# Performance work log

Measured on AMD Instinct MI355X. Metric: run time of the kernel, lower is better.

The kernel has to match this reference:

```python
import jax, jax.numpy as jnp
import numpy as np

N_ENT = 50000
N_REL = 1000
D_E = 32
D_R = 32
RANK = 40
B = 64
EPS = 1e-5


def _bn(x, gamma, beta):
    # BatchNorm1d in training mode: biased batch stats over the batch dim
    mu = x.mean(axis=0)
    var = x.var(axis=0)
    return (x - mu) * jax.lax.rsqrt(var + EPS) * gamma + beta


def setup_inputs() -> dict:
    key = jax.random.key(0)
    ks = jax.random.split(key, 10)
    E_weight = jax.random.normal(ks[0], (N_ENT, D_E), jnp.float32) * 0.001
    E_weight = E_weight.at[0].set(0.0)  # padding_idx=0
    R_weight = jax.random.normal(ks[1], (N_REL, D_R), jnp.float32) * 0.001
    R_weight = R_weight.at[0].set(0.0)
    ht_left = jax.random.normal(ks[2], (RANK, D_E, D_E), jnp.float32) * 0.1
    ht_right = jax.random.normal(ks[3], (RANK, D_E, D_E), jnp.float32) * 0.1
    ht_internal = jax.random.normal(ks[4], (RANK, RANK, RANK), jnp.float32) * 0.1
    ht_root = jax.random.normal(ks[5], (D_R, RANK), jnp.float32) * 0.1
    r_idx = jax.random.randint(ks[6], (B,), 0, N_REL)
    e_idx = jax.random.randint(ks[7], (3, B), 0, N_ENT)
    return {
        "E_weight": E_weight, "R_weight": R_weight,
        "ht_left": ht_left, "ht_right": ht_right,
        "ht_internal": ht_internal, "ht_root": ht_root,
        "bne_gamma": jnp.ones(D_E), "bne_beta": jnp.zeros(D_E),
        "bnr_gamma": jnp.ones(D_R), "bnr_beta": jnp.zeros(D_R),
        "bnw_gamma": jnp.ones(D_E), "bnw_beta": jnp.zeros(D_E),
        "r_idx": r_idx, "e_idx": e_idx, "miss_ent_domain": 1,
    }


def reference(E_weight, R_weight, ht_left, ht_right, ht_internal, ht_root,
              bne_gamma, bne_beta, bnr_gamma, bnr_beta, bnw_gamma, bnw_beta,
              r_idx, e_idx, miss_ent_domain):
    d_r = R_weight.shape[1]
    d_e = E_weight.shape[1]
    # build_W: HT contraction to full 5-D core W[d,i,j,k,l]
    W_int = jnp.einsum('cab,aij,bkl->cijkl', ht_internal, ht_left, ht_right)
    W = jnp.einsum('dc,cijkl->dijkl', ht_root, W_int)
    # relation-conditioned core
    r_emb = _bn(R_weight[r_idx], bnr_gamma, bnr_beta)           # [B, d_r]
    W_mat = (r_emb @ W.reshape(d_r, -1)).reshape(-1, d_e, d_e, d_e, d_e)
    # known entity embeddings (dropout = 0)
    es = [_bn(E_weight[e_idx[i]], bne_gamma, bne_beta) for i in range(3)]
    eq = {1: 'bijkl,bj,bk,bl->bi', 2: 'bijkl,bi,bk,bl->bj',
          3: 'bijkl,bi,bj,bl->bk', 4: 'bijkl,bi,bj,bk->bl'}[int(miss_ent_domain)]
    W_out = jnp.einsum(eq, W_mat, *es)                          # [B, d_e]
    W_out = _bn(W_out, bnw_gamma, bnw_beta)
    pred = jax.nn.softmax(W_out @ E_weight.T, axis=1)           # [B, n_ent]
    return (pred, W)
```

## Files before the change

### kernel.cpp

```cpp
#include <hip/hip_runtime.h>

#define N_ENT 50000
#define D_E 32
#define RANK 40
#define NB 64
#define EPS 1e-5f

#define GN (32 * RANK * RANK)
#define GBLK ((GN + 255) / 256)
#define WBLK 1024
#define LBLK ((N_ENT + 255) / 256)
#define NXCH 25

typedef float f32x4 __attribute__((ext_vector_type(4)));


__global__ __launch_bounds__(256) void k_prep(
    const float* __restrict__ Ew, const float* __restrict__ Rw,
    const float* __restrict__ L, const float* __restrict__ Rt,
    const float* __restrict__ internal, const float* __restrict__ root,
    const float* __restrict__ bne_g, const float* __restrict__ bne_b,
    const float* __restrict__ bnr_g, const float* __restrict__ bnr_b,
    const int* __restrict__ r_idx, const int* __restrict__ e_idx,
    const int* __restrict__ dom_p,
    float* __restrict__ G, float* __restrict__ wraw)
{
    int t = threadIdx.x;
    int blk = blockIdx.x;
    if (blk >= NB) {
        int idx = (blk - NB) * 256 + t;
        if (idx < GN) {
            int d  = idx / (RANK * RANK);
            int ab = idx - d * (RANK * RANK);
            float acc = 0.f;
            #pragma unroll 8
            for (int c = 0; c < RANK; ++c)
                acc += root[d * RANK + c] * internal[c * RANK * RANK + ab];
            G[idx] = acc;
        }
        return;
    }
    int bb = blk;
    int dom = *dom_p;
    __shared__ float sTab[4][NB][32];
    __shared__ float sMu[4][32], sRs[4][32], sBt[4][32];
    __shared__ float sRow[4][32];
    __shared__ float sRc_[RANK];
    __shared__ float sGr[RANK * RANK];
    __shared__ float sv[RANK], sg[RANK];
    __shared__ float sX[RANK * 32];

    for (int e = t; e < NB * 32; e += 256) {
        int r = e >> 5, c = e & 31;
        sTab[0][r][c] = Rw[r_idx[r] * 32 + c];
        sTab[1][r][c] = Ew[(size_t)e_idx[r] * 32 + c];
        sTab[2][r][c] = Ew[(size_t)e_idx[NB + r] * 32 + c];
        sTab[3][r][c] = Ew[(size_t)e_idx[2 * NB + r] * 32 + c];
    }
    __syncthreads();
    if (t < 128) {
        int tb = t >> 5, c = t & 31;
        float s = 0.f;
        for (int r = 0; r < NB; ++r) s += sTab[tb][r][c];
        float mean = s * (1.f / NB);
        float v = 0.f;
        for (int r = 0; r < NB; ++r) { float d = sTab[tb][r][c] - mean; v += d * d; }
        v *= (1.f / NB);
        const float* gm = (tb == 0) ? bnr_g : bne_g;
        const float* bt = (tb == 0) ? bnr_b : bne_b;
        sMu[tb][c] = mean;
        sRs[tb][c] = gm[c] / sqrtf(v + EPS);
        sBt[tb][c] = bt[c];
    }
    __syncthreads();
    if (t < 128) {
        int tb = t >> 5, c = t & 31;
        sRow[tb][c] = (sTab[tb][bb][c] - sMu[tb][c]) * sRs[tb][c] + sBt[tb][c];
    }
    __syncthreads();
    if (t < RANK) {
        float acc = 0.f;
        #pragma unroll 8
        for (int d = 0; d < 32; ++d) acc += sRow[0][d] * root[d * RANK + t];
        sRc_[t] = acc;
    }
    const float* s0 = sRow[1];
    const float* s1 = sRow[2];
    const float* s2 = sRow[3];
    if (dom <= 2) {
        if (t < RANK) {
            float acc = 0.f;
            for (int k = 0; k < 32; ++k) {
                float inner = 0.f;
                #pragma unroll 8
                for (int l = 0; l < 32; ++l) inner += Rt[t * 1024 + k * 32 + l] * s2[l];
                acc += inner * s1[k];
            }
            sv[t] = acc;
        }
        for (int e = t; e < RANK * 32; e += 256) {
            int a = e >> 5, o = e & 31;
            float acc = 0.f;
            if (dom == 1) { for (int j = 0; j < 32; ++j) acc += L[a * 1024 + o * 32 + j] * s0[j]; }
            else          { for (int i = 0; i < 32; ++i) acc += L[a * 1024 + i * 32 + o] * s0[i]; }
            sX[e] = acc;
        }
    } else {
        if (t < RANK) {
            float acc = 0.f;
            for (int i = 0; i < 32; ++i) {
                float inner = 0.f;
                #pragma unroll 8
                for (int j = 0; j < 32; ++j) inner += L[t * 1024 + i * 32 + j] * s1[j];
                acc += inner * s0[i];
            }
            sv[t] = acc;
        }
        for (int e = t; e < RANK * 32; e += 256) {
            int b2 = e >> 5, o = e & 31;
            float acc = 0.f;
            if (dom == 3) { for (int l = 0; l < 32; ++l) acc += Rt[b2 * 1024 + o * 32 + l] * s2[l]; }
            else          { for (int k = 0; k < 32; ++k) acc += Rt[b2 * 1024 + k * 32 + o] * s1[k]; }
            sX[e] = acc;
        }
    }
    __syncthreads();
    for (int e = t; e < RANK * RANK; e += 256) {
        float acc = 0.f;
        #pragma unroll 8
        for (int c = 0; c < RANK; ++c) acc += sRc_[c] * internal[c * RANK * RANK + e];
        sGr[e] = acc;
    }
    __syncthreads();
    if (t < RANK) {
        float acc = 0.f;
        if (dom <= 2) { for (int b2 = 0; b2 < RANK; ++b2) acc += sGr[t * RANK + b2] * sv[b2]; }
        else          { for (int a = 0; a < RANK; ++a)   acc += sGr[a * RANK + t] * sv[a]; }
        sg[t] = acc;
    }
    __syncthreads();
    if (t < 32) {
        float acc = 0.f;
        for (int x = 0; x < RANK; ++x) acc += sg[x] * sX[x * 32 + t];
        wraw[bb * 32 + t] = acc;
    }
}

__global__ __launch_bounds__(256) void k_main(
    const float* __restrict__ G, const float* __restrict__ L,
    const float* __restrict__ Rt, const float* __restrict__ E,
    const float* __restrict__ wraw,
    const float* __restrict__ bnw_g, const float* __restrict__ bnw_b,
    float* __restrict__ W, float* __restrict__ pred, float* __restrict__ psum)
{
    __shared__ float smem[6400];
    int t = threadIdx.x;
    if (blockIdx.x < WBLK) {
        float* sT  = smem;
        float* sRc = smem + 1280;
        int blk = blockIdx.x, d = blk >> 5, i = blk & 31;
        for (int e = t; e < RANK * 32; e += 256) {
            int b2 = e >> 5, j = e & 31;
            float acc = 0.f;
            #pragma unroll 8
            for (int a = 0; a < RANK; ++a)
                acc += G[d * (RANK * RANK) + a * RANK + b2] * L[a * 1024 + i * 32 + j];
            sT[b2 * 32 + j] = acc;
        }
        int jg  = (t >> 5) << 2;
        int kq4 = (t & 31) << 2;
        float* Wrow = W + (size_t)blk * 32 * 1024;
        const f32x4* R4 = (const f32x4*)Rt;
        f32x4* sRc4 = (f32x4*)sRc;
        for (int ch = 0; ch < 8; ++ch) {
            __syncthreads();
            for (int e = t; e < RANK * 32; e += 256) {
                int b2 = e >> 5, x = e & 31;
                sRc4[b2 * 32 + x] = R4[b2 * 256 + ch * 32 + x];
            }
            __syncthreads();
            float acc[4][4] = {};
            #pragma unroll 4
            for (int b2 = 0; b2 < RANK; ++b2) {
                f32x4 tv = *(const f32x4*)&sT[b2 * 32 + jg];
                f32x4 rv = *(const f32x4*)&sRc[b2 * 128 + kq4];
                acc[0][0] += tv.x * rv.x; acc[0][1] += tv.x * rv.y; acc[0][2] += tv.x * rv.z; acc[0][3] += tv.x * rv.w;
                acc[1][0] += tv.y * rv.x; acc[1][1] += tv.y * rv.y; acc[1][2] += tv.y * rv.z; acc[1][3] += tv.y * rv.w;
                acc[2][0] += tv.z * rv.x; acc[2][1] += tv.z * rv.y; acc[2][2] += tv.z * rv.z; acc[2][3] += tv.z * rv.w;
                acc[3][0] += tv.w * rv.x; acc[3][1] += tv.w * rv.y; acc[3][2] += tv.w * rv.z; acc[3][3] += tv.w * rv.w;
            }
            #pragma unroll
            for (int jy = 0; jy < 4; ++jy) {
                f32x4 o = { acc[jy][0], acc[jy][1], acc[jy][2], acc[jy][3] };
                __builtin_nontemporal_store(o, (f32x4*)&Wrow[(size_t)(jg + jy) * 1024 + ch * 128 + kq4]);
            }
        }
    } else {
        int chunk = blockIdx.x - WBLK;
        float* wbn  = smem;
        float* sacc = smem + 2048;
        float* sst  = smem + 2304;
        for (int e = t; e < 2048; e += 256) wbn[e] = wraw[e];
        __syncthreads();
        if (t < 32) {
            float s = 0.f;
            for (int r = 0; r < NB; ++r) s += wbn[r * 32 + t];
            float mean = s * (1.f / NB);
            float v = 0.f;
            for (int r = 0; r < NB; ++r) { float d = wbn[r * 32 + t] - mean; v += d * d; }
            v *= (1.f / NB);
            sst[t]      = mean;
            sst[32 + t] = bnw_g[t] / sqrtf(v + EPS);
            sst[64 + t] = bnw_b[t];
        }
        __syncthreads();
        for (int e = t; e < 2048; e += 256) {
            int c = e & 31;
            wbn[e] = (wbn[e] - sst[c]) * sst[32 + c] + sst[64 + c];
        }
        __syncthreads();
        int ent = chunk * 256 + t;
        bool valid = ent < N_ENT;
        float er[32];
        if (valid) {
            const f32x4* Er = (const f32x4*)(E + (size_t)ent * 32);
            #pragma unroll
            for (int q = 0; q < 8; ++q) {
                f32x4 v4 = Er[q];
                er[q * 4 + 0] = v4.x; er[q * 4 + 1] = v4.y;
                er[q * 4 + 2] = v4.z; er[q * 4 + 3] = v4.w;
            }
        } else {
            #pragma unroll
            for (int q = 0; q < 32; ++q) er[q] = 0.f;
        }
        int wv = t >> 6;
        for (int b = 0; b < NB; ++b) {
            float s = 0.f;
            #pragma unroll
            for (int p = 0; p < 32; ++p) s += wbn[b * 32 + p] * er[p];
            if (valid) pred[(size_t)b * N_ENT + ent] = s;
            float pz = valid ? __expf(s) : 0.f;
            #pragma unroll
            for (int off = 32; off >= 1; off >>= 1) pz += __shfl_xor(pz, off);
            if ((t & 63) == 0) sacc[wv * 64 + b] = pz;
        }
        __syncthreads();
        if (t < NB)
            psum[chunk * NB + t] = sacc[t] + sacc[64 + t] + sacc[128 + t] + sacc[192 + t];
    }
}

__global__ __launch_bounds__(256) void k_normexp(
    float* __restrict__ pred, const float* __restrict__ psum)
{
    int b = blockIdx.y, cx = blockIdx.x, t = threadIdx.x;
    __shared__ float sred[4];
    __shared__ float sinv;
    float v = (t < LBLK) ? psum[t * NB + b] : 0.f;
    #pragma unroll
    for (int off = 32; off >= 1; off >>= 1) v += __shfl_xor(v, off);
    if ((t & 63) == 0) sred[t >> 6] = v;
    __syncthreads();
    if (t == 0) sinv = 1.f / (sred[0] + sred[1] + sred[2] + sred[3]);
    __syncthreads();
    float inv = sinv;
    f32x4* p4 = (f32x4*)pred + (size_t)b * (N_ENT / 4);
    #pragma unroll
    for (int q = 0; q < 2; ++q) {
        int f = cx * 512 + q * 256 + t;
        if (f < N_ENT / 4) {
            f32x4 x = p4[f];
            x.x = __expf(x.x) * inv; x.y = __expf(x.y) * inv;
            x.z = __expf(x.z) * inv; x.w = __expf(x.w) * inv;
            p4[f] = x;
        }
    }
}

extern "C" void kernel_launch(void* const* d_in, const int* in_sizes, int n_in,
                              void* d_out, int out_size, void* d_ws, size_t ws_size,
                              hipStream_t stream) {
    const float* E_weight = (const float*)d_in[0];
    const float* R_weight = (const float*)d_in[1];
    const float* ht_left  = (const float*)d_in[2];
    const float* ht_right = (const float*)d_in[3];
    const float* ht_int   = (const float*)d_in[4];
    const float* ht_root  = (const float*)d_in[5];
    const float* bne_g = (const float*)d_in[6];
    const float* bne_b = (const float*)d_in[7];
    const float* bnr_g = (const float*)d_in[8];
    const float* bnr_b = (const float*)d_in[9];
    const float* bnw_g = (const float*)d_in[10];
    const float* bnw_b = (const float*)d_in[11];
    const int* r_idx = (const int*)d_in[12];
    const int* e_idx = (const int*)d_in[13];
    const int* dom   = (const int*)d_in[14];

    float* ws   = (float*)d_ws;
    float* G    = ws;
    float* wraw = ws + 51200;
    float* psum = ws + 53248;

    float* pred = (float*)d_out;
    float* Wout = (float*)d_out + (size_t)NB * N_ENT;

    k_prep<<<NB + GBLK, 256, 0, stream>>>(E_weight, R_weight, ht_left, ht_right,
                                          ht_int, ht_root, bne_g, bne_b, bnr_g, bnr_b,
                                          r_idx, e_idx, dom, G, wraw);
    k_main<<<WBLK + LBLK, 256, 0, stream>>>(G, ht_left, ht_right, E_weight, wraw,
                                            bnw_g, bnw_b, Wout, pred, psum);
    {
        dim3 g(NXCH, NB);
        k_normexp<<<g, 256, 0, stream>>>(pred, psum);
    }
}
```

Baseline: 122.2 us.

## Build W with bf16 MFMA and recompute logits instead of storing pred twice

The W core is now formed with 32x32x16 bf16 MFMA instructions. The ht_right factor is pre-packed into a bf16 fragment layout in the prep kernel, and the per-block T tile is converted to bf16 in shared memory. The softmax path no longer writes raw logits and reads them back. The middle kernel only produces exp partial sums, and a final kernel recomputes the logits from E, applies exp and normalisation, and writes pred once. This removes a full read-modify-write of the 12.8MB pred array, at the cost of recomputing the dot products and reducing W's precision to bf16 inputs, which may exceed the tolerance.

```diff
diff --git a/kernel.cpp b/kernel.cpp
--- a/kernel.cpp
+++ b/kernel.cpp
@@ -1,19 +1,26 @@
 #include <hip/hip_runtime.h>
 
 #define N_ENT 50000
-#define D_E 32
 #define RANK 40
 #define NB 64
 #define EPS 1e-5f
 
 #define GN (32 * RANK * RANK)
-#define GBLK ((GN + 255) / 256)
+#define GBLK 200
+#define RFBLK 32
 #define WBLK 1024
-#define LBLK ((N_ENT + 255) / 256)
-#define NXCH 25
-
-typedef float f32x4 __attribute__((ext_vector_type(4)));
-
+#define LBLK 196
+
+typedef float f32x4  __attribute__((ext_vector_type(4)));
+typedef float f32x16 __attribute__((ext_vector_type(16)));
+typedef short s16x8  __attribute__((ext_vector_type(8)));
+
+
+__device__ __forceinline__ unsigned short f2bf(float f) {
+    unsigned u = __float_as_uint(f);
+    u += 0x7FFF + ((u >> 16) & 1);
+    return (unsigned short)(u >> 16);
+}
 
 __global__ __launch_bounds__(256) void k_prep(
     const float* __restrict__ Ew, const float* __restrict__ Rw,
@@ -23,10 +30,24 @@
     const float* __restrict__ bnr_g, const float* __restrict__ bnr_b,
     const int* __restrict__ r_idx, const int* __restrict__ e_idx,
     const int* __restrict__ dom_p,
-    float* __restrict__ G, float* __restrict__ wraw)
+    float* __restrict__ G, float* __restrict__ wraw,
+    unsigned short* __restrict__ RfU)
 {
     int t = threadIdx.x;
     int blk = blockIdx.x;
+    if (blk >= NB + GBLK) {
+        int nt = blk - (NB + GBLK);
+        for (int e = t; e < 1536; e += 256) {
+            int i  = e & 7;
+            int l  = (e >> 3) & 63;
+            int ks = e >> 9;
+            int b  = 16 * ks + 8 * (l >> 5) + i;
+            int n  = nt * 32 + (l & 31);
+            float v = (b < RANK) ? Rt[b * 1024 + n] : 0.f;
+            RfU[((nt * 3 + ks) * 64 + l) * 8 + i] = f2bf(v);
+        }
+        return;
+    }
     if (blk >= NB) {
         int idx = (blk - NB) * 256 + t;
         if (idx < GN) {
@@ -146,57 +167,77 @@
     }
 }
 
-__global__ __launch_bounds__(256) void k_main(
+__global__ __launch_bounds__(256) void k_mid(
     const float* __restrict__ G, const float* __restrict__ L,
-    const float* __restrict__ Rt, const float* __restrict__ E,
-    const float* __restrict__ wraw,
+    const float* __restrict__ E, const float* __restrict__ wraw,
     const float* __restrict__ bnw_g, const float* __restrict__ bnw_b,
-    float* __restrict__ W, float* __restrict__ pred, float* __restrict__ psum)
+    const unsigned short* __restrict__ RfU,
+    float* __restrict__ W, float* __restrict__ wbn_out, float* __restrict__ psum)
 {
-    __shared__ float smem[6400];
+    __shared__ float smem[4736];
     int t = threadIdx.x;
-    if (blockIdx.x < WBLK) {
-        float* sT  = smem;
-        float* sRc = smem + 1280;
-        int blk = blockIdx.x, d = blk >> 5, i = blk & 31;
-        for (int e = t; e < RANK * 32; e += 256) {
-            int b2 = e >> 5, j = e & 31;
-            float acc = 0.f;
-            #pragma unroll 8
-            for (int a = 0; a < RANK; ++a)
-                acc += G[d * (RANK * RANK) + a * RANK + b2] * L[a * 1024 + i * 32 + j];
-            sT[b2 * 32 + j] = acc;
-        }
-        int jg  = (t >> 5) << 2;
-        int kq4 = (t & 31) << 2;
-        float* Wrow = W + (size_t)blk * 32 * 1024;
-        const f32x4* R4 = (const f32x4*)Rt;
-        f32x4* sRc4 = (f32x4*)sRc;
-        for (int ch = 0; ch < 8; ++ch) {
-            __syncthreads();
-            for (int e = t; e < RANK * 32; e += 256) {
-                int b2 = e >> 5, x = e & 31;
-                sRc4[b2 * 32 + x] = R4[b2 * 256 + ch * 32 + x];
-            }
-            __syncthreads();
-            float acc[4][4] = {};
-            #pragma unroll 4
-            for (int b2 = 0; b2 < RANK; ++b2) {
-                f32x4 tv = *(const f32x4*)&sT[b2 * 32 + jg];
-                f32x4 rv = *(const f32x4*)&sRc[b2 * 128 + kq4];
-                acc[0][0] += tv.x * rv.x; acc[0][1] += tv.x * rv.y; acc[0][2] += tv.x * rv.z; acc[0][3] += tv.x * rv.w;
-                acc[1][0] += tv.y * rv.x; acc[1][1] += tv.y * rv.y; acc[1][2] += tv.y * rv.z; acc[1][3] += tv.y * rv.w;
-                acc[2][0] += tv.z * rv.x; acc[2][1] += tv.z * rv.y; acc[2][2] += tv.z * rv.z; acc[2][3] += tv.z * rv.w;
-                acc[3][0] += tv.w * rv.x; acc[3][1] += tv.w * rv.y; acc[3][2] += tv.w * rv.z; acc[3][3] += tv.w * rv.w;
-            }
-            #pragma unroll
-            for (int jy = 0; jy < 4; ++jy) {
-                f32x4 o = { acc[jy][0], acc[jy][1], acc[jy][2], acc[jy][3] };
-                __builtin_nontemporal_store(o, (f32x4*)&Wrow[(size_t)(jg + jy) * 1024 + ch * 128 + kq4]);
+    if (blockIdx.x >= LBLK) {
+        int blk = blockIdx.x - LBLK;
+        int d = blk >> 5, i = blk & 31;
+        float* sG = smem;
+        float* sL = smem + 1920;
+        unsigned short* Tb = (unsigned short*)(smem + 3200);
+        for (int e = t; e < 1920; e += 256) {
+            int a = e / 48, b = e - a * 48;
+            sG[e] = (b < RANK) ? G[d * (RANK * RANK) + a * RANK + b] : 0.f;
+        }
+        for (int e = t; e < 1280; e += 256)
+            sL[e] = L[(e >> 5) * 1024 + i * 32 + (e & 31)];
+        __syncthreads();
+        if (t < 192) {
+            int j = t / 6, g = t - (t / 6) * 6, b0 = g * 8;
+            float acc8[8] = {0.f, 0.f, 0.f, 0.f, 0.f, 0.f, 0.f, 0.f};
+            for (int a = 0; a < RANK; ++a) {
+                float lj = sL[a * 32 + j];
+                f32x4 g0 = *(const f32x4*)&sG[a * 48 + b0];
+                f32x4 g1 = *(const f32x4*)&sG[a * 48 + b0 + 4];
+                acc8[0] += lj * g0.x; acc8[1] += lj * g0.y;
+                acc8[2] += lj * g0.z; acc8[3] += lj * g0.w;
+                acc8[4] += lj * g1.x; acc8[5] += lj * g1.y;
+                acc8[6] += lj * g1.z; acc8[7] += lj * g1.w;
+            }
+            s16x8 pk;
+            pk[0] = (short)f2bf(acc8[0]); pk[1] = (short)f2bf(acc8[1]);
+            pk[2] = (short)f2bf(acc8[2]); pk[3] = (short)f2bf(acc8[3]);
+            pk[4] = (short)f2bf(acc8[4]); pk[5] = (short)f2bf(acc8[5]);
+            pk[6] = (short)f2bf(acc8[6]); pk[7] = (short)f2bf(acc8[7]);
+            *(s16x8*)&Tb[(g * 32 + j) * 8] = pk;
+        }
+        __syncthreads();
+        int l = t & 63, w = t >> 6;
+        int coln = l & 31;
+        int rowb = 4 * (l >> 5);
+        const s16x8* Rf8 = (const s16x8*)RfU;
+        const s16x8* Tb8 = (const s16x8*)Tb;
+        float* Wrow = W + (size_t)blk * 32768;
+        s16x8 af0 = Tb8[(0 * 2 + (l >> 5)) * 32 + coln];
+        s16x8 af1 = Tb8[(1 * 2 + (l >> 5)) * 32 + coln];
+        s16x8 af2 = Tb8[(2 * 2 + (l >> 5)) * 32 + coln];
+        #pragma unroll 2
+        for (int it = 0; it < 8; ++it) {
+            int nt = w * 8 + it;
+            s16x8 bf0 = Rf8[(nt * 3 + 0) * 64 + l];
+            s16x8 bf1 = Rf8[(nt * 3 + 1) * 64 + l];
+            s16x8 bf2 = Rf8[(nt * 3 + 2) * 64 + l];
+            f32x16 acc = {0.f,0.f,0.f,0.f,0.f,0.f,0.f,0.f,
+                          0.f,0.f,0.f,0.f,0.f,0.f,0.f,0.f};
+            acc = __builtin_amdgcn_mfma_f32_32x32x16_bf16(af0, bf0, acc, 0, 0, 0);
+            acc = __builtin_amdgcn_mfma_f32_32x32x16_bf16(af1, bf1, acc, 0, 0, 0);
+            acc = __builtin_amdgcn_mfma_f32_32x32x16_bf16(af2, bf2, acc, 0, 0, 0);
+            float* outp = Wrow + (size_t)rowb * 1024 + nt * 32 + coln;
+            #pragma unroll
+            for (int q = 0; q < 16; ++q) {
+                int j = (q & 3) + 8 * (q >> 2);
+                __builtin_nontemporal_store(acc[q], outp + (size_t)j * 1024);
             }
         }
     } else {
-        int chunk = blockIdx.x - WBLK;
+        int blk = blockIdx.x;
         float* wbn  = smem;
         float* sacc = smem + 2048;
         float* sst  = smem + 2304;
@@ -219,7 +260,9 @@
             wbn[e] = (wbn[e] - sst[c]) * sst[32 + c] + sst[64 + c];
         }
         __syncthreads();
-        int ent = chunk * 256 + t;
+        if (blk == 0)
+            for (int e = t; e < 2048; e += 256) wbn_out[e] = wbn[e];
+        int ent = blk * 256 + t;
         bool valid = ent < N_ENT;
         float er[32];
         if (valid) {
@@ -238,8 +281,11 @@
         for (int b = 0; b < NB; ++b) {
             float s = 0.f;
             #pragma unroll
-            for (int p = 0; p < 32; ++p) s += wbn[b * 32 + p] * er[p];
-            if (valid) pred[(size_t)b * N_ENT + ent] = s;
+            for (int p = 0; p < 8; ++p) {
+                f32x4 wv4 = *(const f32x4*)&wbn[b * 32 + p * 4];
+                s += wv4.x * er[p * 4] + wv4.y * er[p * 4 + 1]
+                   + wv4.z * er[p * 4 + 2] + wv4.w * er[p * 4 + 3];
+            }
             float pz = valid ? __expf(s) : 0.f;
             #pragma unroll
             for (int off = 32; off >= 1; off >>= 1) pz += __shfl_xor(pz, off);
@@ -247,34 +293,54 @@
         }
         __syncthreads();
         if (t < NB)
-            psum[chunk * NB + t] = sacc[t] + sacc[64 + t] + sacc[128 + t] + sacc[192 + t];
-    }
-}
-
-__global__ __launch_bounds__(256) void k_normexp(
-    float* __restrict__ pred, const float* __restrict__ psum)
+            psum[blk * NB + t] = sacc[t] + sacc[64 + t] + sacc[128 + t] + sacc[192 + t];
+    }
+}
+
+__global__ __launch_bounds__(256) void k_final(
+    const float* __restrict__ E, const float* __restrict__ wbn_in,
+    const float* __restrict__ psum, float* __restrict__ pred)
 {
-    int b = blockIdx.y, cx = blockIdx.x, t = threadIdx.x;
-    __shared__ float sred[4];
-    __shared__ float sinv;
-    float v = (t < LBLK) ? psum[t * NB + b] : 0.f;
-    #pragma unroll
-    for (int off = 32; off >= 1; off >>= 1) v += __shfl_xor(v, off);
-    if ((t & 63) == 0) sred[t >> 6] = v;
-    __syncthreads();
-    if (t == 0) sinv = 1.f / (sred[0] + sred[1] + sred[2] + sred[3]);
-    __syncthreads();
-    float inv = sinv;
-    f32x4* p4 = (f32x4*)pred + (size_t)b * (N_ENT / 4);
-    #pragma unroll
-    for (int q = 0; q < 2; ++q) {
-        int f = cx * 512 + q * 256 + t;
-        if (f < N_ENT / 4) {
-            f32x4 x = p4[f];
-            x.x = __expf(x.x) * inv; x.y = __expf(x.y) * inv;
-            x.z = __expf(x.z) * inv; x.w = __expf(x.w) * inv;
-            p4[f] = x;
-        }
+    __shared__ float swbn[2048];
+    __shared__ float spart[4][64];
+    __shared__ float sinv[64];
+    int t = threadIdx.x;
+    for (int e = t; e < 2048; e += 256) swbn[e] = wbn_in[e];
+    {
+        int b = t & 63, part = t >> 6;
+        float s = 0.f;
+        for (int c = part; c < LBLK; c += 4) s += psum[c * NB + b];
+        spart[part][b] = s;
+    }
+    __syncthreads();
+    if (t < NB)
+        sinv[t] = 1.f / (spart[0][t] + spart[1][t] + spart[2][t] + spart[3][t]);
+    __syncthreads();
+    int ent = blockIdx.x * 256 + t;
+    bool valid = ent < N_ENT;
+    float er[32];
+    if (valid) {
+        const f32x4* Er = (const f32x4*)(E + (size_t)ent * 32);
+        #pragma unroll
+        for (int q = 0; q < 8; ++q) {
+            f32x4 v4 = Er[q];
+            er[q * 4 + 0] = v4.x; er[q * 4 + 1] = v4.y;
+            er[q * 4 + 2] = v4.z; er[q * 4 + 3] = v4.w;
+        }
+    } else {
+        #pragma unroll
+        for (int q = 0; q < 32; ++q) er[q] = 0.f;
+    }
+    for (int b = 0; b < NB; ++b) {
+        float s = 0.f;
+        #pragma unroll
+        for (int p = 0; p < 8; ++p) {
+            f32x4 wv4 = *(const f32x4*)&swbn[b * 32 + p * 4];
+            s += wv4.x * er[p * 4] + wv4.y * er[p * 4 + 1]
+               + wv4.z * er[p * 4 + 2] + wv4.w * er[p * 4 + 3];
+        }
+        if (valid)
+            __builtin_nontemporal_store(__expf(s) * sinv[b], &pred[(size_t)b * N_ENT + ent]);
     }
 }
 
@@ -300,18 +366,17 @@
     float* ws   = (float*)d_ws;
     float* G    = ws;
     float* wraw = ws + 51200;
-    float* psum = ws + 53248;
+    float* wbn  = ws + 53248;
+    float* psum = ws + 55296;
+    unsigned short* RfU = (unsigned short*)(ws + 67840);
 
     float* pred = (float*)d_out;
     float* Wout = (float*)d_out + (size_t)NB * N_ENT;
 
-    k_prep<<<NB + GBLK, 256, 0, stream>>>(E_weight, R_weight, ht_left, ht_right,
-                                          ht_int, ht_root, bne_g, bne_b, bnr_g, bnr_b,
-                                          r_idx, e_idx, dom, G, wraw);
-    k_main<<<WBLK + LBLK, 256, 0, stream>>>(G, ht_left, ht_right, E_weight, wraw,
-                                            bnw_g, bnw_b, Wout, pred, psum);
-    {
-        dim3 g(NXCH, NB);
-        k_normexp<<<g, 256, 0, stream>>>(pred, psum);
-    }
-}
+    k_prep<<<NB + GBLK + RFBLK, 256, 0, stream>>>(E_weight, R_weight, ht_left, ht_right,
+                                                  ht_int, ht_root, bne_g, bne_b, bnr_g, bnr_b,
+                                                  r_idx, e_idx, dom, G, wraw, RfU);
+    k_mid<<<LBLK + WBLK, 256, 0, stream>>>(G, ht_left, E_weight, wraw,
+                                           bnw_g, bnw_b, RfU, Wout, wbn, psum);
+    k_final<<<LBLK, 256, 0, stream>>>(E_weight, wbn, psum, pred);
+}
```

Result: faster. 114.9 us (-6.0%).
